# Kernel tuning notes

Measured on AMD Instinct MI355X. Metric: run time of the kernel, lower is better.

Reference implementation:

```python
import jax, jax.numpy as jnp
import numpy as np

D = 1024
H = 16
DH = D // H  # 64

def setup_inputs() -> dict:
    key = jax.random.key(0)
    ks = jax.random.split(key, 9)
    B, L = 2, 2048
    s = 1.0 / np.sqrt(D)
    inp = {
        'x':  jax.random.normal(ks[0], (B, L, D), dtype=jnp.float32),
        'Wq': jax.random.uniform(ks[1], (D, D), jnp.float32, -s, s),
        'bq': jnp.zeros((D,), jnp.float32),
        'Wk': jax.random.uniform(ks[2], (D, D), jnp.float32, -s, s),
        'bk': jnp.zeros((D,), jnp.float32),
        'Wv': jax.random.uniform(ks[3], (D, D), jnp.float32, -s, s),
        'bv': jnp.zeros((D,), jnp.float32),
        'Wo': jax.random.uniform(ks[4], (D, D), jnp.float32, -s, s),
        'bo': jnp.zeros((D,), jnp.float32),
    }
    return inp

def reference(x, Wq, bq, Wk, bk, Wv, bv, Wo, bo):
    B, L, _ = x.shape
    # projections (torch Linear: x @ W.T + b; here weights stored as [D_in, D_out])
    q = (x @ Wq + bq).reshape(B, L, H, DH).transpose(0, 2, 1, 3)  # [B,H,L,DH]
    k = (x @ Wk + bk).reshape(B, L, H, DH).transpose(0, 2, 1, 3)
    v = (x @ Wv + bv).reshape(B, L, H, DH).transpose(0, 2, 1, 3)
    scores = jnp.einsum('bhqd,bhkd->bhqk', q, k) / jnp.sqrt(jnp.float32(DH))
    attn = jax.nn.softmax(scores, axis=-1)  # dropout p=0 / eval -> identity
    out = jnp.einsum('bhqk,bhkd->bhqd', attn, v)
    out = out.transpose(0, 2, 1, 3).reshape(B, L, D)
    return out @ Wo + bo
```

## Files before the change

kernel.cpp:

```cpp
#include <hip/hip_runtime.h>
#include <stdint.h>

typedef __attribute__((ext_vector_type(8)))  __bf16 bf16x8;
typedef __attribute__((ext_vector_type(4)))  __bf16 bf16x4;
typedef __attribute__((ext_vector_type(4)))  float  f32x4;
typedef __attribute__((ext_vector_type(16))) float  f32x16;
typedef __attribute__((ext_vector_type(4)))  int    i32x4;

#define DEV static __device__ __forceinline__

DEV float fast_exp2(float x) {
#if __has_builtin(__builtin_amdgcn_exp2f)
  return __builtin_amdgcn_exp2f(x);
#else
  return exp2f(x);
#endif
}

DEV uint32_t pack_bf2(float a, float b) {
  __bf16 x = (__bf16)a, y = (__bf16)b;
  uint16_t xu = __builtin_bit_cast(uint16_t, x);
  uint16_t yu = __builtin_bit_cast(uint16_t, y);
  return (uint32_t)xu | ((uint32_t)yu << 16);
}

DEV void gload_lds16(const void* g, void* l) {
  __builtin_amdgcn_global_load_lds(
      (const __attribute__((address_space(1))) void*)(uintptr_t)(g),
      (__attribute__((address_space(3))) void*)(uint32_t)(uintptr_t)(l),
      16, 0, 0);
}

#define SM_SCALE 0.18033688f

__global__ void k_prep(const float* __restrict__ x,  __bf16* __restrict__ xb,
                       const float* __restrict__ Wq, const float* __restrict__ Wk,
                       const float* __restrict__ Wv, const float* __restrict__ Wo,
                       __bf16* __restrict__ wtq, __bf16* __restrict__ wot) {
  const int z = blockIdx.z;
  if (z < 4) {
    const float* W  = (z == 0) ? Wq : (z == 1) ? Wk : (z == 2) ? Wv : Wo;
    __bf16*      Wt = (z == 3) ? wot : (wtq + (size_t)z * 1024 * 1024);
    __shared__ __bf16 T[64][66];
    int t = threadIdx.x;
    int r = t >> 2;
    int cq = (t & 3) << 4;
    {
      int gk = blockIdx.y * 64 + r;
      int gn0 = blockIdx.x * 64 + cq;
      const float* src = W + (size_t)gk * 1024 + gn0;
#pragma unroll
      for (int j = 0; j < 16; j += 4) {
        f32x4 v = *(const f32x4*)(src + j);
#pragma unroll
        for (int jj = 0; jj < 4; ++jj) T[r][cq + j + jj] = (__bf16)v[jj];
      }
    }
    __syncthreads();
    {
      int gn = blockIdx.x * 64 + r;
      int gk0 = blockIdx.y * 64 + cq;
      __bf16* dst = Wt + (size_t)gn * 1024 + gk0;
      bf16x8 o0, o1;
#pragma unroll
      for (int j = 0; j < 8; ++j) { o0[j] = T[cq + j][r]; o1[j] = T[cq + 8 + j][r]; }
      *(bf16x8*)dst = o0;
      *(bf16x8*)(dst + 8) = o1;
    }
  } else {
    int lb = (z - 4) * 256 + blockIdx.y * 16 + blockIdx.x;
    int i = (lb * 256 + (int)threadIdx.x) * 4;
    if (i < 4096 * 1024) {
      f32x4 v = *(const f32x4*)(x + i);
      bf16x4 o;
      o[0] = (__bf16)v[0]; o[1] = (__bf16)v[1];
      o[2] = (__bf16)v[2]; o[3] = (__bf16)v[3];
      *(bf16x4*)(xb + i) = o;
    }
  }
}

__global__ void k_vt(const __bf16* __restrict__ qkv, __bf16* __restrict__ Vt) {
  __shared__ __bf16 T[64][66];
  int lt = blockIdx.x, bh = blockIdx.y;
  int b = bh >> 4, h = bh & 15;
  int t = threadIdx.x;
  int r = t >> 2, cq = (t & 3) << 4;
  {
    const __bf16* src = qkv + (size_t)(b * 2048 + lt * 64 + r) * 3072 + 2048 + h * 64 + cq;
    bf16x8 v0 = *(const bf16x8*)src;
    bf16x8 v1 = *(const bf16x8*)(src + 8);
#pragma unroll
    for (int j = 0; j < 8; ++j) { T[r][cq + j] = v0[j]; T[r][cq + 8 + j] = v1[j]; }
  }
  __syncthreads();
  {
    __bf16* dst = Vt + (size_t)(bh * 64 + r) * 2048 + lt * 64 + cq;
    bf16x8 o0, o1;
#pragma unroll
    for (int j = 0; j < 8; ++j) { o0[j] = T[cq + j][r]; o1[j] = T[cq + 8 + j][r]; }
    *(bf16x8*)dst = o0;
    *(bf16x8*)(dst + 8) = o1;
  }
}

template <int OUTMODE>
__global__ void k_gemm(const __bf16* __restrict__ A, const __bf16* __restrict__ Bt,
                       void* __restrict__ Cout, int M, int N, int K,
                       const float* __restrict__ b0, const float* __restrict__ b1,
                       const float* __restrict__ b2) {
  __shared__ __align__(16) __bf16 As[128 * 64];
  __shared__ __align__(16) __bf16 Bs[128 * 64];
  const int t = threadIdx.x, wid = t >> 6, lane = t & 63;
  const int bm = blockIdx.y, bn = blockIdx.x;
  const int wm = wid >> 1, wn = wid & 1;
  const int l15 = lane & 15, l4 = lane >> 4;
  const int rr = lane >> 3, cc = lane & 7;
  f32x4 acc[4][4] = {};
  const int nk = K >> 6;
  for (int kt = 0; kt < nk; ++kt) {
    __syncthreads();
#pragma unroll
    for (int j = 0; j < 4; ++j) {
      int row = wid * 32 + j * 8 + rr;
      int csrc = (cc ^ (row & 7)) * 8;
      gload_lds16(A + (size_t)(bm * 128 + row) * K + kt * 64 + csrc,
                  (char*)As + (wid * 32 + j * 8) * 128);
      gload_lds16(Bt + (size_t)(bn * 128 + row) * K + kt * 64 + csrc,
                  (char*)Bs + (wid * 32 + j * 8) * 128);
    }
    __syncthreads();
#pragma unroll
    for (int kk = 0; kk < 2; ++kk) {
      bf16x8 a[4], b[4];
#pragma unroll
      for (int ms = 0; ms < 4; ++ms) {
        int row = wm * 64 + ms * 16 + l15;
        a[ms] = *(const bf16x8*)((char*)As + row * 128 + (((kk * 4 + l4) ^ (row & 7)) * 16));
      }
#pragma unroll
      for (int ns = 0; ns < 4; ++ns) {
        int row = wn * 64 + ns * 16 + l15;
        b[ns] = *(const bf16x8*)((char*)Bs + row * 128 + (((kk * 4 + l4) ^ (row & 7)) * 16));
      }
#pragma unroll
      for (int ms = 0; ms < 4; ++ms)
#pragma unroll
        for (int ns = 0; ns < 4; ++ns)
          acc[ms][ns] = __builtin_amdgcn_mfma_f32_16x16x32_bf16(a[ms], b[ns], acc[ms][ns], 0, 0, 0);
    }
  }
#pragma unroll
  for (int ms = 0; ms < 4; ++ms) {
#pragma unroll
    for (int ns = 0; ns < 4; ++ns) {
      int n = bn * 128 + wn * 64 + ns * 16 + l15;
      float bias;
      if (OUTMODE == 0) {
        const float* bp = (n < 1024) ? b0 : ((n < 2048) ? b1 : b2);
        bias = bp[n & 1023];
      } else {
        bias = b0[n];
      }
#pragma unroll
      for (int i = 0; i < 4; ++i) {
        int m = bm * 128 + wm * 64 + ms * 16 + l4 * 4 + i;
        float v = acc[ms][ns][i] + bias;
        if (OUTMODE == 0) {
          if (n < 1024) v *= SM_SCALE;
          ((__bf16*)Cout)[(size_t)m * N + n] = (__bf16)v;
        } else {
          ((float*)Cout)[(size_t)m * N + n] = v;
        }
      }
    }
  }
}

__global__ void __launch_bounds__(512, 2)
k_attn(const __bf16* __restrict__ qkv, const __bf16* __restrict__ Vt,
       __bf16* __restrict__ Aout) {
  __shared__ __align__(16) char smem[65536];
  const int t = threadIdx.x, w = t >> 6, lane = t & 63;
  const int wq = w & 3, half = w >> 2;
  const int l31 = lane & 31, hi = lane >> 5;
  const int f = blockIdx.x;
  const int qt = (f >> 3) & 15;
  const int bh = (f & 7) + 8 * (f >> 7);
  const int b = bh >> 4, h = bh & 15;
  const int kv0 = half * 1024;

  const __bf16* Kg = qkv + (size_t)(b * 2048) * 3072 + 1024 + h * 64;
  const __bf16* Vg = Vt + (size_t)(bh * 64) * 2048;

  bf16x8 aq[4];
  {
    int qrow = b * 2048 + qt * 128 + wq * 32 + l31;
    const __bf16* qp = qkv + (size_t)qrow * 3072 + h * 64 + hi * 8;
#pragma unroll
    for (int d = 0; d < 4; ++d) aq[d] = *(const bf16x8*)(qp + d * 16);
  }

  f32x16 o[2] = {};
  float ls[16];
#pragma unroll
  for (int r = 0; r < 16; ++r) ls[r] = 0.f;

  auto STAGE = [&](int bi, int kt) {
    char* Kl = smem + half * 32768 + bi * 16384;
    char* Vl = Kl + 8192;
    const __bf16* kg = Kg + (size_t)(kv0 + kt * 64) * 3072;
    const __bf16* vg = Vg + (kv0 + kt * 64);
#pragma unroll
    for (int jj = 0; jj < 2; ++jj) {
      int idx = (wq * 2 + jj) * 64 + lane;
      int row = (idx >> 8) * 32 + (idx & 31);
      int col = ((idx >> 5) & 7) * 8;
      gload_lds16(kg + (size_t)row * 3072 + col, Kl + (wq * 2 + jj) * 1024);
      gload_lds16(vg + (size_t)row * 2048 + col, Vl + (wq * 2 + jj) * 1024);
    }
  };

  STAGE(0, 0);
  __syncthreads();

  int cur = 0;
  for (int kt = 0; kt < 16; ++kt) {
    if (kt < 15) STAGE(cur ^ 1, kt + 1);
    char* Kl = smem + half * 32768 + cur * 16384;
    char* Vl = Kl + 8192;
    const char* Kv = Kl + lane * 16;
    const char* Vv = Vl + lane * 16;

    f32x16 s[2];
    s[0] = 0.f; s[1] = 0.f;
    __builtin_amdgcn_s_setprio(1);
#pragma unroll
    for (int ks = 0; ks < 2; ++ks)
#pragma unroll
      for (int d = 0; d < 4; ++d) {
        bf16x8 kf = *(const bf16x8*)(Kv + ks * 4096 + d * 1024);
        s[ks] = __builtin_amdgcn_mfma_f32_32x32x16_bf16(kf, aq[d], s[ks], 0, 0, 0);
      }
    __builtin_amdgcn_s_setprio(0);

#pragma unroll
    for (int ks = 0; ks < 2; ++ks)
#pragma unroll
      for (int r = 0; r < 16; ++r)
        s[ks][r] = fast_exp2(s[ks][r]);

#pragma unroll
    for (int r = 0; r < 16; ++r) ls[r] += s[0][r] + s[1][r];

    uint32_t W[2][8];
#pragma unroll
    for (int ks = 0; ks < 2; ++ks)
#pragma unroll
      for (int c = 0; c < 8; ++c)
        W[ks][c] = pack_bf2(s[ks][2 * c], s[ks][2 * c + 1]);

    bf16x8 pa[4];
#pragma unroll
    for (int kstep = 0; kstep < 4; ++kstep) {
      const int ks = kstep >> 1, base = 4 * (kstep & 1);
      uint32_t w0 = W[ks][base + 0], w1 = W[ks][base + 1];
      uint32_t w2 = W[ks][base + 2], w3 = W[ks][base + 3];
      uint32_t x0 = __shfl_xor((int)w0, 32);
      uint32_t x1 = __shfl_xor((int)w1, 32);
      uint32_t x2 = __shfl_xor((int)w2, 32);
      uint32_t x3 = __shfl_xor((int)w3, 32);
      i32x4 pw;
      pw[0] = (int)(hi ? x2 : w0);
      pw[1] = (int)(hi ? x3 : w1);
      pw[2] = (int)(hi ? w2 : x0);
      pw[3] = (int)(hi ? w3 : x1);
      pa[kstep] = __builtin_bit_cast(bf16x8, pw);
    }

    __builtin_amdgcn_s_setprio(1);
#pragma unroll
    for (int kstep = 0; kstep < 4; ++kstep)
#pragma unroll
      for (int db = 0; db < 2; ++db) {
        bf16x8 vf = *(const bf16x8*)(Vv + db * 4096 + kstep * 1024);
        o[db] = __builtin_amdgcn_mfma_f32_32x32x16_bf16(pa[kstep], vf, o[db], 0, 0, 0);
      }
    __builtin_amdgcn_s_setprio(0);

    __syncthreads();
    cur ^= 1;
  }

#pragma unroll
  for (int st = 8; st > 0; st >>= 1)
#pragma unroll
    for (int r = 0; r < st; ++r) ls[r] += ls[r + st];
  float rowsum = ls[0] + __shfl_xor(ls[0], 32);

  float* oLDS = (float*)smem;
  float* sLDS = (float*)(smem + 32768);
  sLDS[w * 64 + lane] = rowsum;
  if (w >= 4) {
    float* ob = oLDS + (w - 4) * 2048;
#pragma unroll
    for (int db = 0; db < 2; ++db)
#pragma unroll
      for (int r = 0; r < 16; ++r)
        ob[(db * 16 + r) * 64 + lane] = o[db][r];
  }
  __syncthreads();
  if (w < 4) {
#pragma unroll
    for (int r = 0; r < 16; ++r) {
      int rowq = (r & 3) + 8 * (r >> 2) + 4 * hi;
      float rs1 = __shfl(rowsum, rowq);
      float rs2 = sLDS[(w + 4) * 64 + rowq];
      float inv = 1.0f / (rs1 + rs2);
      int qg = b * 2048 + qt * 128 + wq * 32 + rowq;
#pragma unroll
      for (int db = 0; db < 2; ++db) {
        float o2 = oLDS[w * 2048 + (db * 16 + r) * 64 + lane];
        float v = (o[db][r] + o2) * inv;
        int col = h * 64 + db * 32 + l31;
        Aout[(size_t)qg * 1024 + col] = (__bf16)v;
      }
    }
  }
}

extern "C" void kernel_launch(void* const* d_in, const int* in_sizes, int n_in,
                              void* d_out, int out_size, void* d_ws, size_t ws_size,
                              hipStream_t stream) {
  const float* x  = (const float*)d_in[0];
  const float* Wq = (const float*)d_in[1];
  const float* bq = (const float*)d_in[2];
  const float* Wk = (const float*)d_in[3];
  const float* bk = (const float*)d_in[4];
  const float* Wv = (const float*)d_in[5];
  const float* bv = (const float*)d_in[6];
  const float* Wo = (const float*)d_in[7];
  const float* bo = (const float*)d_in[8];
  float* out = (float*)d_out;

  char* ws = (char*)d_ws;
  __bf16* xb   = (__bf16*)(ws);
  __bf16* wtq  = (__bf16*)(ws + (8ull  << 20));
  __bf16* wot  = (__bf16*)(ws + (14ull << 20));
  __bf16* qkv  = (__bf16*)(ws + (16ull << 20));
  __bf16* vt   = (__bf16*)(ws + (40ull << 20));
  __bf16* aout = (__bf16*)(ws + (48ull << 20));

  k_prep<<<dim3(16, 16, 20), 256, 0, stream>>>(x, xb, Wq, Wk, Wv, Wo, wtq, wot);

  k_gemm<0><<<dim3(24, 32), 256, 0, stream>>>(xb, wtq, qkv, 4096, 3072, 1024, bq, bk, bv);

  k_vt<<<dim3(32, 32), 256, 0, stream>>>(qkv, vt);

  k_attn<<<dim3(512), 512, 0, stream>>>(qkv, vt, aout);

  k_gemm<1><<<dim3(8, 32), 256, 0, stream>>>(aout, wot, out, 4096, 1024, 1024, bo, nullptr, nullptr);
}
```

Before: 117.2 us.

## Split attention KV range four ways with smaller blocks and tree reduction

The attention kernel now processes 64 queries per block, with four wave-quarters each handling a 512-key slice in 32-key tiles, and launches twice as many blocks. It uses a smaller single-buffered LDS footprint and a higher launch-bounds occupancy target. It drops the double-buffered prefetch in favour of load-then-sync per tile, and merges the partial outputs and row sums through a two-level LDS reduction. The aim is more parallelism and occupancy, at the cost of exposed load latency, an extra barrier per tile and a longer final reduction.

```diff
diff --git a/kernel.cpp b/kernel.cpp
--- a/kernel.cpp
+++ b/kernel.cpp
@@ -177,95 +177,87 @@
   }
 }
 
-__global__ void __launch_bounds__(512, 2)
+__global__ void __launch_bounds__(512, 6)
 k_attn(const __bf16* __restrict__ qkv, const __bf16* __restrict__ Vt,
        __bf16* __restrict__ Aout) {
-  __shared__ __align__(16) char smem[65536];
+  __shared__ __align__(16) char smem[33792];
   const int t = threadIdx.x, w = t >> 6, lane = t & 63;
-  const int wq = w & 3, half = w >> 2;
+  const int quarter = w & 3, qsub = w >> 2;
   const int l31 = lane & 31, hi = lane >> 5;
   const int f = blockIdx.x;
-  const int qt = (f >> 3) & 15;
-  const int bh = (f & 7) + 8 * (f >> 7);
+  const int qt = (f >> 3) & 31;
+  const int bh = (f & 7) + 8 * (f >> 8);
   const int b = bh >> 4, h = bh & 15;
-  const int kv0 = half * 1024;
+  const int kv0 = quarter * 512;
 
   const __bf16* Kg = qkv + (size_t)(b * 2048) * 3072 + 1024 + h * 64;
   const __bf16* Vg = Vt + (size_t)(bh * 64) * 2048;
 
   bf16x8 aq[4];
   {
-    int qrow = b * 2048 + qt * 128 + wq * 32 + l31;
+    int qrow = b * 2048 + qt * 64 + qsub * 32 + l31;
     const __bf16* qp = qkv + (size_t)qrow * 3072 + h * 64 + hi * 8;
 #pragma unroll
     for (int d = 0; d < 4; ++d) aq[d] = *(const bf16x8*)(qp + d * 16);
   }
 
   f32x16 o[2] = {};
-  float ls[16];
-#pragma unroll
-  for (int r = 0; r < 16; ++r) ls[r] = 0.f;
-
-  auto STAGE = [&](int bi, int kt) {
-    char* Kl = smem + half * 32768 + bi * 16384;
-    char* Vl = Kl + 8192;
-    const __bf16* kg = Kg + (size_t)(kv0 + kt * 64) * 3072;
-    const __bf16* vg = Vg + (kv0 + kt * 64);
-#pragma unroll
-    for (int jj = 0; jj < 2; ++jj) {
-      int idx = (wq * 2 + jj) * 64 + lane;
-      int row = (idx >> 8) * 32 + (idx & 31);
-      int col = ((idx >> 5) & 7) * 8;
-      gload_lds16(kg + (size_t)row * 3072 + col, Kl + (wq * 2 + jj) * 1024);
-      gload_lds16(vg + (size_t)row * 2048 + col, Vl + (wq * 2 + jj) * 1024);
-    }
-  };
-
-  STAGE(0, 0);
-  __syncthreads();
-
-  int cur = 0;
+  float lsum = 0.f;
+
+  char* Kl = smem + quarter * 8192;
+  char* Vl = Kl + 4096;
+
   for (int kt = 0; kt < 16; ++kt) {
-    if (kt < 15) STAGE(cur ^ 1, kt + 1);
-    char* Kl = smem + half * 32768 + cur * 16384;
-    char* Vl = Kl + 8192;
+    __syncthreads();
+    {
+      const __bf16* kg = Kg + (size_t)(kv0 + kt * 32) * 3072;
+      const __bf16* vg = Vg + (kv0 + kt * 32);
+#pragma unroll
+      for (int j = 0; j < 2; ++j) {
+        int g = qsub * 2 + j;
+        gload_lds16(kg + (size_t)l31 * 3072 + (g * 2 + hi) * 8, Kl + g * 1024);
+        gload_lds16(vg + (size_t)((g & 1) * 32 + l31) * 2048 + ((g >> 1) * 2 + hi) * 8,
+                    Vl + g * 1024);
+      }
+    }
+    __syncthreads();
     const char* Kv = Kl + lane * 16;
     const char* Vv = Vl + lane * 16;
 
-    f32x16 s[2];
-    s[0] = 0.f; s[1] = 0.f;
+    f32x16 s;
+    s = 0.f;
     __builtin_amdgcn_s_setprio(1);
 #pragma unroll
-    for (int ks = 0; ks < 2; ++ks)
-#pragma unroll
-      for (int d = 0; d < 4; ++d) {
-        bf16x8 kf = *(const bf16x8*)(Kv + ks * 4096 + d * 1024);
-        s[ks] = __builtin_amdgcn_mfma_f32_32x32x16_bf16(kf, aq[d], s[ks], 0, 0, 0);
-      }
+    for (int d = 0; d < 4; ++d) {
+      bf16x8 kf = *(const bf16x8*)(Kv + d * 1024);
+      s = __builtin_amdgcn_mfma_f32_32x32x16_bf16(kf, aq[d], s, 0, 0, 0);
+    }
     __builtin_amdgcn_s_setprio(0);
 
 #pragma unroll
-    for (int ks = 0; ks < 2; ++ks)
-#pragma unroll
-      for (int r = 0; r < 16; ++r)
-        s[ks][r] = fast_exp2(s[ks][r]);
-
-#pragma unroll
-    for (int r = 0; r < 16; ++r) ls[r] += s[0][r] + s[1][r];
-
-    uint32_t W[2][8];
-#pragma unroll
-    for (int ks = 0; ks < 2; ++ks)
-#pragma unroll
-      for (int c = 0; c < 8; ++c)
-        W[ks][c] = pack_bf2(s[ks][2 * c], s[ks][2 * c + 1]);
-
-    bf16x8 pa[4];
-#pragma unroll
-    for (int kstep = 0; kstep < 4; ++kstep) {
-      const int ks = kstep >> 1, base = 4 * (kstep & 1);
-      uint32_t w0 = W[ks][base + 0], w1 = W[ks][base + 1];
-      uint32_t w2 = W[ks][base + 2], w3 = W[ks][base + 3];
+    for (int r = 0; r < 16; ++r) s[r] = fast_exp2(s[r]);
+
+    {
+      float u[8];
+#pragma unroll
+      for (int c = 0; c < 8; ++c) u[c] = s[2 * c] + s[2 * c + 1];
+#pragma unroll
+      for (int st = 4; st > 0; st >>= 1)
+#pragma unroll
+        for (int c = 0; c < st; ++c) u[c] += u[c + st];
+      lsum += u[0];
+    }
+
+    uint32_t W[8];
+#pragma unroll
+    for (int c = 0; c < 8; ++c) W[c] = pack_bf2(s[2 * c], s[2 * c + 1]);
+
+    bf16x8 pa[2];
+#pragma unroll
+    for (int kstep = 0; kstep < 2; ++kstep) {
+      const int base = 4 * kstep;
+      uint32_t w0 = W[base + 0], w1 = W[base + 1];
+      uint32_t w2 = W[base + 2], w3 = W[base + 3];
       uint32_t x0 = __shfl_xor((int)w0, 32);
       uint32_t x1 = __shfl_xor((int)w1, 32);
       uint32_t x2 = __shfl_xor((int)w2, 32);
@@ -280,50 +272,71 @@
 
     __builtin_amdgcn_s_setprio(1);
 #pragma unroll
-    for (int kstep = 0; kstep < 4; ++kstep)
+    for (int kstep = 0; kstep < 2; ++kstep)
 #pragma unroll
       for (int db = 0; db < 2; ++db) {
-        bf16x8 vf = *(const bf16x8*)(Vv + db * 4096 + kstep * 1024);
+        bf16x8 vf = *(const bf16x8*)(Vv + (kstep * 2 + db) * 1024);
         o[db] = __builtin_amdgcn_mfma_f32_32x32x16_bf16(pa[kstep], vf, o[db], 0, 0, 0);
       }
     __builtin_amdgcn_s_setprio(0);
-
-    __syncthreads();
-    cur ^= 1;
-  }
-
-#pragma unroll
-  for (int st = 8; st > 0; st >>= 1)
-#pragma unroll
-    for (int r = 0; r < st; ++r) ls[r] += ls[r + st];
-  float rowsum = ls[0] + __shfl_xor(ls[0], 32);
+  }
+
+  lsum += __shfl_xor(lsum, 32);
 
   float* oLDS = (float*)smem;
   float* sLDS = (float*)(smem + 32768);
-  sLDS[w * 64 + lane] = rowsum;
-  if (w >= 4) {
-    float* ob = oLDS + (w - 4) * 2048;
+  __syncthreads();
+  if (quarter >= 2) {
+    int slot = (quarter - 2) * 2 + qsub;
+    float* ob = oLDS + slot * 2048;
 #pragma unroll
     for (int db = 0; db < 2; ++db)
 #pragma unroll
       for (int r = 0; r < 16; ++r)
         ob[(db * 16 + r) * 64 + lane] = o[db][r];
+    sLDS[slot * 64 + lane] = lsum;
   }
   __syncthreads();
-  if (w < 4) {
+  if (quarter < 2) {
+    int slot = quarter * 2 + qsub;
+    const float* ob = oLDS + slot * 2048;
+#pragma unroll
+    for (int db = 0; db < 2; ++db)
+#pragma unroll
+      for (int r = 0; r < 16; ++r)
+        o[db][r] += ob[(db * 16 + r) * 64 + lane];
+    lsum += sLDS[slot * 64 + lane];
+  }
+  if (quarter == 1) {
+    int slot = 2 + qsub;
+    float* ob = oLDS + slot * 2048;
+#pragma unroll
+    for (int db = 0; db < 2; ++db)
+#pragma unroll
+      for (int r = 0; r < 16; ++r)
+        ob[(db * 16 + r) * 64 + lane] = o[db][r];
+    sLDS[slot * 64 + lane] = lsum;
+  }
+  __syncthreads();
+  if (quarter == 0) {
+    int slot = 2 + qsub;
+    const float* ob = oLDS + slot * 2048;
+#pragma unroll
+    for (int db = 0; db < 2; ++db)
+#pragma unroll
+      for (int r = 0; r < 16; ++r)
+        o[db][r] += ob[(db * 16 + r) * 64 + lane];
+    lsum += sLDS[slot * 64 + lane];
+
 #pragma unroll
     for (int r = 0; r < 16; ++r) {
       int rowq = (r & 3) + 8 * (r >> 2) + 4 * hi;
-      float rs1 = __shfl(rowsum, rowq);
-      float rs2 = sLDS[(w + 4) * 64 + rowq];
-      float inv = 1.0f / (rs1 + rs2);
-      int qg = b * 2048 + qt * 128 + wq * 32 + rowq;
+      float inv = 1.0f / __shfl(lsum, rowq);
+      int qg = b * 2048 + qt * 64 + qsub * 32 + rowq;
 #pragma unroll
       for (int db = 0; db < 2; ++db) {
-        float o2 = oLDS[w * 2048 + (db * 16 + r) * 64 + lane];
-        float v = (o[db][r] + o2) * inv;
         int col = h * 64 + db * 32 + l31;
-        Aout[(size_t)qg * 1024 + col] = (__bf16)v;
+        Aout[(size_t)qg * 1024 + col] = (__bf16)(o[db][r] * inv);
       }
     }
   }
@@ -357,7 +370,7 @@
 
   k_vt<<<dim3(32, 32), 256, 0, stream>>>(qkv, vt);
 
-  k_attn<<<dim3(512), 512, 0, stream>>>(qkv, vt, aout);
+  k_attn<<<dim3(1024), 512, 0, stream>>>(qkv, vt, aout);
 
   k_gemm<1><<<dim3(8, 32), 256, 0, stream>>>(aout, wot, out, 4096, 1024, 1024, bo, nullptr, nullptr);
 }
```

Result: slower. 181.2 us (+54.6%).
